# Optimization experiments

Hardware: AMD Instinct MI355X
Metric: run time of the kernel (lower is better)

The kernel has to match this reference:

```python
import jax, jax.numpy as jnp
import numpy as np

JITTER_NOISE = 0.01  # matches init_kwargs jitter_noise


def setup_inputs() -> dict:
    key = jax.random.key(0)
    k1, k2, k3 = jax.random.split(key, 3)
    G, T, D, E = 8, 4096, 2048, 64
    token_inputs = jax.random.normal(k1, (G, T, D), dtype=jnp.float32)
    noise = jax.random.uniform(k2, (G, T, D), dtype=jnp.float32)  # U[0,1), rescaled in reference
    weight = jax.random.normal(k3, (E, D), dtype=jnp.float32) * 0.02  # nn.init.normal_(std=0.02)
    bias = jnp.zeros((E,), dtype=jnp.float32)
    return {"token_inputs": token_inputs, "noise": noise, "weight": weight,
            "bias": bias, "expert_capacity": 128}


def reference(token_inputs, noise, weight, bias, expert_capacity):
    # Jitter: torch uniform_(1 - j, 1 + j) applied multiplicatively
    x = token_inputs * (1.0 - JITTER_NOISE + 2.0 * JITTER_NOISE * noise)
    # Router logits: Linear(dim -> num_experts)
    logits = jnp.einsum('gtd,ed->gte', x, weight) + bias  # [G, T, E]
    probs = jax.nn.softmax(logits, axis=-1)
    # ignore_padding_tokens: zero logits of all-zero tokens
    padding_mask = (jnp.sum(jnp.abs(x), axis=-1) > 0)[..., None]  # [G, T, 1]
    masked_logits = logits * padding_mask
    # Router z-loss on (masked) logits
    log_z = jax.nn.logsumexp(masked_logits, axis=-1)  # [G, T]
    G, T, _ = masked_logits.shape
    z_loss = jnp.sum(log_z ** 2) / (G * T)
    return probs, masked_logits, z_loss
```

## Files before the change

### kernel.cpp

```cpp
#include <hip/hip_runtime.h>
#include <math.h>

#define G_   8
#define T_   4096
#define D_   2048
#define E_   64
#define ROWS (G_*T_)
#define BM   64
#define BK   32
#define NIT  (D_/BK)

__global__ __launch_bounds__(256) void router_kernel(
    const float* __restrict__ tok,
    const float* __restrict__ noi,
    const float* __restrict__ wgt,
    const float* __restrict__ bias,
    float* __restrict__ probs,
    float* __restrict__ masked,
    float* __restrict__ zloss)
{
    __shared__ float xs[BK][BM];
    __shared__ float ws[BK][E_];
    __shared__ float abs_row[BM];
    __shared__ float zred[4];

    const int tid  = threadIdx.x;
    const int lrow = tid >> 2;
    const int lc   = tid & 3;
    const int ty   = tid >> 4;
    const int tx   = tid & 15;
    const size_t row0 = (size_t)blockIdx.x * BM;

    const float* tbase = tok + (row0 + (size_t)lrow) * D_ + lc * 4;
    const float* nbase = noi + (row0 + (size_t)lrow) * D_ + lc * 4;
    const float* wbase = wgt + (size_t)lrow * D_ + lc * 4;

    float acc[4][4];
#pragma unroll
    for (int i = 0; i < 4; ++i)
#pragma unroll
        for (int j = 0; j < 4; ++j) acc[i][j] = 0.f;
    float absacc = 0.f;

    float4 a0 = *(const float4*)(tbase +  0);
    float4 a1 = *(const float4*)(tbase + 16);
    float4 n0 = *(const float4*)(nbase +  0);
    float4 n1 = *(const float4*)(nbase + 16);
    float4 w0 = *(const float4*)(wbase +  0);
    float4 w1 = *(const float4*)(wbase + 16);

    for (int it = 0; it < NIT; ++it) {
        float4 x0, x1;
        x0.x = a0.x * (0.99f + 0.02f * n0.x);
        x0.y = a0.y * (0.99f + 0.02f * n0.y);
        x0.z = a0.z * (0.99f + 0.02f * n0.z);
        x0.w = a0.w * (0.99f + 0.02f * n0.w);
        x1.x = a1.x * (0.99f + 0.02f * n1.x);
        x1.y = a1.y * (0.99f + 0.02f * n1.y);
        x1.z = a1.z * (0.99f + 0.02f * n1.z);
        x1.w = a1.w * (0.99f + 0.02f * n1.w);
        absacc += fabsf(x0.x) + fabsf(x0.y) + fabsf(x0.z) + fabsf(x0.w)
                + fabsf(x1.x) + fabsf(x1.y) + fabsf(x1.z) + fabsf(x1.w);

        xs[lc*4+0 ][lrow] = x0.x;  xs[lc*4+1 ][lrow] = x0.y;
        xs[lc*4+2 ][lrow] = x0.z;  xs[lc*4+3 ][lrow] = x0.w;
        xs[lc*4+16][lrow] = x1.x;  xs[lc*4+17][lrow] = x1.y;
        xs[lc*4+18][lrow] = x1.z;  xs[lc*4+19][lrow] = x1.w;
        ws[lc*4+0 ][lrow] = w0.x;  ws[lc*4+1 ][lrow] = w0.y;
        ws[lc*4+2 ][lrow] = w0.z;  ws[lc*4+3 ][lrow] = w0.w;
        ws[lc*4+16][lrow] = w1.x;  ws[lc*4+17][lrow] = w1.y;
        ws[lc*4+18][lrow] = w1.z;  ws[lc*4+19][lrow] = w1.w;
        __syncthreads();

        {
            int knext = (it + 1 < NIT) ? (it + 1) * BK : it * BK;
            a0 = *(const float4*)(tbase + knext);
            a1 = *(const float4*)(tbase + knext + 16);
            n0 = *(const float4*)(nbase + knext);
            n1 = *(const float4*)(nbase + knext + 16);
            w0 = *(const float4*)(wbase + knext);
            w1 = *(const float4*)(wbase + knext + 16);
        }

#pragma unroll 8
        for (int k = 0; k < BK; ++k) {
            float4 av = *(const float4*)&xs[k][ty*4];
            float4 bv = *(const float4*)&ws[k][tx*4];
            float aa[4] = {av.x, av.y, av.z, av.w};
            float bb[4] = {bv.x, bv.y, bv.z, bv.w};
#pragma unroll
            for (int i = 0; i < 4; ++i)
#pragma unroll
                for (int j = 0; j < 4; ++j)
                    acc[i][j] = fmaf(aa[i], bb[j], acc[i][j]);
        }
        __syncthreads();
    }

    absacc += __shfl_xor(absacc, 1);
    absacc += __shfl_xor(absacc, 2);
    if (lc == 0) abs_row[lrow] = absacc;
    __syncthreads();

    float bj[4];
#pragma unroll
    for (int j = 0; j < 4; ++j) bj[j] = bias[tx*4 + j];

    float zpart = 0.f;
#pragma unroll
    for (int i = 0; i < 4; ++i) {
        const size_t gr = row0 + (size_t)(ty*4 + i);
        float l[4];
#pragma unroll
        for (int j = 0; j < 4; ++j) l[j] = acc[i][j] + bj[j];

        float m = fmaxf(fmaxf(l[0], l[1]), fmaxf(l[2], l[3]));
        m = fmaxf(m, __shfl_xor(m, 1));
        m = fmaxf(m, __shfl_xor(m, 2));
        m = fmaxf(m, __shfl_xor(m, 4));
        m = fmaxf(m, __shfl_xor(m, 8));

        float e[4]; float s = 0.f;
#pragma unroll
        for (int j = 0; j < 4; ++j) { e[j] = expf(l[j] - m); s += e[j]; }
        s += __shfl_xor(s, 1);
        s += __shfl_xor(s, 2);
        s += __shfl_xor(s, 4);
        s += __shfl_xor(s, 8);
        const float rs = 1.f / s;

        float4 pv = { e[0]*rs, e[1]*rs, e[2]*rs, e[3]*rs };
        *(float4*)(probs + gr * E_ + tx*4) = pv;

        const float msk = (abs_row[ty*4 + i] > 0.f) ? 1.f : 0.f;
        float ml[4];
#pragma unroll
        for (int j = 0; j < 4; ++j) ml[j] = l[j] * msk;
        float4 mv = { ml[0], ml[1], ml[2], ml[3] };
        *(float4*)(masked + gr * E_ + tx*4) = mv;

        float mm = fmaxf(fmaxf(ml[0], ml[1]), fmaxf(ml[2], ml[3]));
        mm = fmaxf(mm, __shfl_xor(mm, 1));
        mm = fmaxf(mm, __shfl_xor(mm, 2));
        mm = fmaxf(mm, __shfl_xor(mm, 4));
        mm = fmaxf(mm, __shfl_xor(mm, 8));
        float ss = 0.f;
#pragma unroll
        for (int j = 0; j < 4; ++j) ss += expf(ml[j] - mm);
        ss += __shfl_xor(ss, 1);
        ss += __shfl_xor(ss, 2);
        ss += __shfl_xor(ss, 4);
        ss += __shfl_xor(ss, 8);
        if (tx == 0) {
            const float lse = mm + logf(ss);
            zpart += lse * lse;
        }
    }

    zpart += __shfl_xor(zpart, 32);
    zpart += __shfl_xor(zpart, 16);
    zpart += __shfl_xor(zpart, 8);
    zpart += __shfl_xor(zpart, 4);
    zpart += __shfl_xor(zpart, 2);
    zpart += __shfl_xor(zpart, 1);
    if ((tid & 63) == 0) zred[tid >> 6] = zpart;
    __syncthreads();
    if (tid == 0) {
        const float z = (zred[0] + zred[1]) + (zred[2] + zred[3]);
        atomicAdd(zloss, z * (1.0f / (float)ROWS));
    }
}

extern "C" void kernel_launch(void* const* d_in, const int* in_sizes, int n_in,
                              void* d_out, int out_size, void* d_ws, size_t ws_size,
                              hipStream_t stream) {
    (void)in_sizes; (void)n_in; (void)ws_size; (void)out_size; (void)d_ws;
    const float* tok  = (const float*)d_in[0];
    const float* noi  = (const float*)d_in[1];
    const float* wgt  = (const float*)d_in[2];
    const float* bias = (const float*)d_in[3];

    float* probs  = (float*)d_out;
    float* masked = probs + (size_t)ROWS * E_;
    float* zloss  = probs + 2 * (size_t)ROWS * E_;

    hipMemsetAsync(zloss, 0, sizeof(float), stream);

    dim3 grid(ROWS / BM);
    dim3 block(256);
    router_kernel<<<grid, block, 0, stream>>>(tok, noi, wgt, bias, probs, masked, zloss);
}
```

Before: 565.0 us.

## Split-K router GEMM with larger 256-row tiles and separate softmax epilogue

Splits the reduction dimension into four slices, each handled by a block computing a 256x64 tile with an 8x8 per-thread register tile. Partial logits and per-row abs sums are accumulated with atomics into the output buffer and a workspace. A second kernel then applies bias, softmax, masking and the z-loss. This raises arithmetic intensity and per-thread ILP, at the cost of float atomics, extra memsets and a second pass over the logits.

```diff
diff --git a/kernel.cpp b/kernel.cpp
--- a/kernel.cpp
+++ b/kernel.cpp
@@ -1,192 +1,221 @@
 #include <hip/hip_runtime.h>
 #include <math.h>
 
-#define G_   8
-#define T_   4096
-#define D_   2048
-#define E_   64
-#define ROWS (G_*T_)
-#define BM   64
-#define BK   32
-#define NIT  (D_/BK)
-
-__global__ __launch_bounds__(256) void router_kernel(
+#define D_    2048
+#define E_    64
+#define ROWS  32768
+#define BM    256
+#define BK    32
+#define KSL   4
+#define KD    (D_/KSL)
+#define NIT   (KD/BK)
+#define XS    260
+#define WSTR  68
+
+__global__ __launch_bounds__(256, 2) void router_gemm(
     const float* __restrict__ tok,
     const float* __restrict__ noi,
     const float* __restrict__ wgt,
+    float* __restrict__ lacc,
+    float* __restrict__ absrow)
+{
+    __shared__ float xs[BK][XS];
+    __shared__ float wsh[BK][WSTR];
+
+    const int tid  = threadIdx.x;
+    const int lane = tid & 63;
+    const int wv   = tid >> 6;
+    const int rowblk = (int)blockIdx.x >> 2;
+    const int ks     = (int)blockIdx.x & 3;
+    const size_t row0 = (size_t)rowblk * BM;
+    const int k0 = ks * KD;
+
+    const int lr  = wv*8 + (lane>>3);
+    const int lko = (lane&7)*4;
+    const float* tptr = tok + (row0 + (size_t)lr)*D_ + (k0 + lko);
+    const float* nptr = noi + (row0 + (size_t)lr)*D_ + (k0 + lko);
+
+    const int we  = tid >> 2;
+    const int wko = (tid & 3) * 8;
+    const float* wptr = wgt + (size_t)we*D_ + (k0 + wko);
+
+    const int ty = tid >> 3;
+    const int tx = tid & 7;
+
+    float acc[8][8];
+#pragma unroll
+    for (int i = 0; i < 8; ++i)
+#pragma unroll
+        for (int j = 0; j < 8; ++j) acc[i][j] = 0.f;
+    float absp[8];
+#pragma unroll
+    for (int p = 0; p < 8; ++p) absp[p] = 0.f;
+
+    float4 ta[8], na[8], wa, wb;
+#pragma unroll
+    for (int p = 0; p < 8; ++p) {
+        ta[p] = *(const float4*)(tptr + (size_t)p*32*D_);
+        na[p] = *(const float4*)(nptr + (size_t)p*32*D_);
+    }
+    wa = *(const float4*)(wptr);
+    wb = *(const float4*)(wptr + 4);
+
+    for (int it = 0; it < NIT; ++it) {
+        __syncthreads();
+
+#pragma unroll
+        for (int p = 0; p < 8; ++p) {
+            const int row = p*32 + lr;
+            const float x0 = ta[p].x * (0.99f + 0.02f * na[p].x);
+            const float x1 = ta[p].y * (0.99f + 0.02f * na[p].y);
+            const float x2 = ta[p].z * (0.99f + 0.02f * na[p].z);
+            const float x3 = ta[p].w * (0.99f + 0.02f * na[p].w);
+            xs[lko+0][row] = x0;
+            xs[lko+1][row] = x1;
+            xs[lko+2][row] = x2;
+            xs[lko+3][row] = x3;
+            absp[p] += fabsf(x0) + fabsf(x1) + fabsf(x2) + fabsf(x3);
+        }
+        {
+            const float* w0 = &wa.x;
+            const float* w1 = &wb.x;
+#pragma unroll
+            for (int j = 0; j < 4; ++j) wsh[wko+j][we]   = w0[j];
+#pragma unroll
+            for (int j = 0; j < 4; ++j) wsh[wko+4+j][we] = w1[j];
+        }
+        __syncthreads();
+
+        {
+            const int itn = (it + 1 < NIT) ? it + 1 : it;
+            const float* tp = tptr + itn*BK;
+            const float* np = nptr + itn*BK;
+            const float* wp = wptr + itn*BK;
+#pragma unroll
+            for (int p = 0; p < 8; ++p) {
+                ta[p] = *(const float4*)(tp + (size_t)p*32*D_);
+                na[p] = *(const float4*)(np + (size_t)p*32*D_);
+            }
+            wa = *(const float4*)(wp);
+            wb = *(const float4*)(wp + 4);
+        }
+
+#pragma unroll 8
+        for (int k = 0; k < BK; ++k) {
+            float4 a0 = *(const float4*)&xs[k][ty*8];
+            float4 a1 = *(const float4*)&xs[k][ty*8+4];
+            float4 b0 = *(const float4*)&wsh[k][tx*8];
+            float4 b1 = *(const float4*)&wsh[k][tx*8+4];
+            float av[8] = {a0.x,a0.y,a0.z,a0.w,a1.x,a1.y,a1.z,a1.w};
+            float bv[8] = {b0.x,b0.y,b0.z,b0.w,b1.x,b1.y,b1.z,b1.w};
+#pragma unroll
+            for (int i = 0; i < 8; ++i)
+#pragma unroll
+                for (int j = 0; j < 8; ++j)
+                    acc[i][j] = fmaf(av[i], bv[j], acc[i][j]);
+        }
+    }
+
+#pragma unroll
+    for (int i = 0; i < 8; ++i) {
+        float* base = lacc + (row0 + (size_t)(ty*8 + i))*E_ + tx*8;
+#pragma unroll
+        for (int j = 0; j < 8; ++j) atomicAdd(base + j, acc[i][j]);
+    }
+
+#pragma unroll
+    for (int p = 0; p < 8; ++p) {
+        float v = absp[p];
+        v += __shfl_xor(v, 1);
+        v += __shfl_xor(v, 2);
+        v += __shfl_xor(v, 4);
+        if ((lane & 7) == 0) atomicAdd(&absrow[row0 + (size_t)(p*32 + lr)], v);
+    }
+}
+
+__global__ __launch_bounds__(256) void router_epi(
     const float* __restrict__ bias,
     float* __restrict__ probs,
-    float* __restrict__ masked,
+    float* __restrict__ lacc,
+    const float* __restrict__ absrow,
     float* __restrict__ zloss)
 {
-    __shared__ float xs[BK][BM];
-    __shared__ float ws[BK][E_];
-    __shared__ float abs_row[BM];
     __shared__ float zred[4];
-
-    const int tid  = threadIdx.x;
-    const int lrow = tid >> 2;
-    const int lc   = tid & 3;
-    const int ty   = tid >> 4;
-    const int tx   = tid & 15;
-    const size_t row0 = (size_t)blockIdx.x * BM;
-
-    const float* tbase = tok + (row0 + (size_t)lrow) * D_ + lc * 4;
-    const float* nbase = noi + (row0 + (size_t)lrow) * D_ + lc * 4;
-    const float* wbase = wgt + (size_t)lrow * D_ + lc * 4;
-
-    float acc[4][4];
-#pragma unroll
-    for (int i = 0; i < 4; ++i)
-#pragma unroll
-        for (int j = 0; j < 4; ++j) acc[i][j] = 0.f;
-    float absacc = 0.f;
-
-    float4 a0 = *(const float4*)(tbase +  0);
-    float4 a1 = *(const float4*)(tbase + 16);
-    float4 n0 = *(const float4*)(nbase +  0);
-    float4 n1 = *(const float4*)(nbase + 16);
-    float4 w0 = *(const float4*)(wbase +  0);
-    float4 w1 = *(const float4*)(wbase + 16);
-
-    for (int it = 0; it < NIT; ++it) {
-        float4 x0, x1;
-        x0.x = a0.x * (0.99f + 0.02f * n0.x);
-        x0.y = a0.y * (0.99f + 0.02f * n0.y);
-        x0.z = a0.z * (0.99f + 0.02f * n0.z);
-        x0.w = a0.w * (0.99f + 0.02f * n0.w);
-        x1.x = a1.x * (0.99f + 0.02f * n1.x);
-        x1.y = a1.y * (0.99f + 0.02f * n1.y);
-        x1.z = a1.z * (0.99f + 0.02f * n1.z);
-        x1.w = a1.w * (0.99f + 0.02f * n1.w);
-        absacc += fabsf(x0.x) + fabsf(x0.y) + fabsf(x0.z) + fabsf(x0.w)
-                + fabsf(x1.x) + fabsf(x1.y) + fabsf(x1.z) + fabsf(x1.w);
-
-        xs[lc*4+0 ][lrow] = x0.x;  xs[lc*4+1 ][lrow] = x0.y;
-        xs[lc*4+2 ][lrow] = x0.z;  xs[lc*4+3 ][lrow] = x0.w;
-        xs[lc*4+16][lrow] = x1.x;  xs[lc*4+17][lrow] = x1.y;
-        xs[lc*4+18][lrow] = x1.z;  xs[lc*4+19][lrow] = x1.w;
-        ws[lc*4+0 ][lrow] = w0.x;  ws[lc*4+1 ][lrow] = w0.y;
-        ws[lc*4+2 ][lrow] = w0.z;  ws[lc*4+3 ][lrow] = w0.w;
-        ws[lc*4+16][lrow] = w1.x;  ws[lc*4+17][lrow] = w1.y;
-        ws[lc*4+18][lrow] = w1.z;  ws[lc*4+19][lrow] = w1.w;
-        __syncthreads();
-
-        {
-            int knext = (it + 1 < NIT) ? (it + 1) * BK : it * BK;
-            a0 = *(const float4*)(tbase + knext);
-            a1 = *(const float4*)(tbase + knext + 16);
-            n0 = *(const float4*)(nbase + knext);
-            n1 = *(const float4*)(nbase + knext + 16);
-            w0 = *(const float4*)(wbase + knext);
-            w1 = *(const float4*)(wbase + knext + 16);
-        }
-
-#pragma unroll 8
-        for (int k = 0; k < BK; ++k) {
-            float4 av = *(const float4*)&xs[k][ty*4];
-            float4 bv = *(const float4*)&ws[k][tx*4];
-            float aa[4] = {av.x, av.y, av.z, av.w};
-            float bb[4] = {bv.x, bv.y, bv.z, bv.w};
-#pragma unroll
-            for (int i = 0; i < 4; ++i)
-#pragma unroll
-                for (int j = 0; j < 4; ++j)
-                    acc[i][j] = fmaf(aa[i], bb[j], acc[i][j]);
-        }
-        __syncthreads();
-    }
-
-    absacc += __shfl_xor(absacc, 1);
-    absacc += __shfl_xor(absacc, 2);
-    if (lc == 0) abs_row[lrow] = absacc;
+    const int tid = threadIdx.x;
+    const int lane = tid & 63;
+    const int wv = tid >> 6;
+    const int r  = tid >> 4;
+    const int tx = tid & 15;
+    const size_t row = (size_t)blockIdx.x*16 + r;
+
+    float4 l4 = *(const float4*)&lacc[row*E_ + tx*4];
+    float l[4] = { l4.x + bias[tx*4+0], l4.y + bias[tx*4+1],
+                   l4.z + bias[tx*4+2], l4.w + bias[tx*4+3] };
+
+    float m = fmaxf(fmaxf(l[0], l[1]), fmaxf(l[2], l[3]));
+    m = fmaxf(m, __shfl_xor(m, 1));
+    m = fmaxf(m, __shfl_xor(m, 2));
+    m = fmaxf(m, __shfl_xor(m, 4));
+    m = fmaxf(m, __shfl_xor(m, 8));
+    float e[4]; float s = 0.f;
+#pragma unroll
+    for (int j = 0; j < 4; ++j) { e[j] = expf(l[j] - m); s += e[j]; }
+    s += __shfl_xor(s, 1);
+    s += __shfl_xor(s, 2);
+    s += __shfl_xor(s, 4);
+    s += __shfl_xor(s, 8);
+    const float rs = 1.f / s;
+    float4 pv = { e[0]*rs, e[1]*rs, e[2]*rs, e[3]*rs };
+    *(float4*)(probs + row*E_ + tx*4) = pv;
+
+    const float msk = (absrow[row] > 0.f) ? 1.f : 0.f;
+    float ml[4] = { l[0]*msk, l[1]*msk, l[2]*msk, l[3]*msk };
+    float4 mv = { ml[0], ml[1], ml[2], ml[3] };
+    *(float4*)(lacc + row*E_ + tx*4) = mv;
+
+    float mm = fmaxf(fmaxf(ml[0], ml[1]), fmaxf(ml[2], ml[3]));
+    mm = fmaxf(mm, __shfl_xor(mm, 1));
+    mm = fmaxf(mm, __shfl_xor(mm, 2));
+    mm = fmaxf(mm, __shfl_xor(mm, 4));
+    mm = fmaxf(mm, __shfl_xor(mm, 8));
+    float ss = 0.f;
+#pragma unroll
+    for (int j = 0; j < 4; ++j) ss += expf(ml[j] - mm);
+    ss += __shfl_xor(ss, 1);
+    ss += __shfl_xor(ss, 2);
+    ss += __shfl_xor(ss, 4);
+    ss += __shfl_xor(ss, 8);
+
+    float zp = 0.f;
+    if (tx == 0) {
+        const float lse = mm + logf(ss);
+        zp = lse * lse;
+    }
+    zp += __shfl_xor(zp, 16);
+    zp += __shfl_xor(zp, 32);
+    if (lane == 0) zred[wv] = zp;
     __syncthreads();
-
-    float bj[4];
-#pragma unroll
-    for (int j = 0; j < 4; ++j) bj[j] = bias[tx*4 + j];
-
-    float zpart = 0.f;
-#pragma unroll
-    for (int i = 0; i < 4; ++i) {
-        const size_t gr = row0 + (size_t)(ty*4 + i);
-        float l[4];
-#pragma unroll
-        for (int j = 0; j < 4; ++j) l[j] = acc[i][j] + bj[j];
-
-        float m = fmaxf(fmaxf(l[0], l[1]), fmaxf(l[2], l[3]));
-        m = fmaxf(m, __shfl_xor(m, 1));
-        m = fmaxf(m, __shfl_xor(m, 2));
-        m = fmaxf(m, __shfl_xor(m, 4));
-        m = fmaxf(m, __shfl_xor(m, 8));
-
-        float e[4]; float s = 0.f;
-#pragma unroll
-        for (int j = 0; j < 4; ++j) { e[j] = expf(l[j] - m); s += e[j]; }
-        s += __shfl_xor(s, 1);
-        s += __shfl_xor(s, 2);
-        s += __shfl_xor(s, 4);
-        s += __shfl_xor(s, 8);
-        const float rs = 1.f / s;
-
-        float4 pv = { e[0]*rs, e[1]*rs, e[2]*rs, e[3]*rs };
-        *(float4*)(probs + gr * E_ + tx*4) = pv;
-
-        const float msk = (abs_row[ty*4 + i] > 0.f) ? 1.f : 0.f;
-        float ml[4];
-#pragma unroll
-        for (int j = 0; j < 4; ++j) ml[j] = l[j] * msk;
-        float4 mv = { ml[0], ml[1], ml[2], ml[3] };
-        *(float4*)(masked + gr * E_ + tx*4) = mv;
-
-        float mm = fmaxf(fmaxf(ml[0], ml[1]), fmaxf(ml[2], ml[3]));
-        mm = fmaxf(mm, __shfl_xor(mm, 1));
-        mm = fmaxf(mm, __shfl_xor(mm, 2));
-        mm = fmaxf(mm, __shfl_xor(mm, 4));
-        mm = fmaxf(mm, __shfl_xor(mm, 8));
-        float ss = 0.f;
-#pragma unroll
-        for (int j = 0; j < 4; ++j) ss += expf(ml[j] - mm);
-        ss += __shfl_xor(ss, 1);
-        ss += __shfl_xor(ss, 2);
-        ss += __shfl_xor(ss, 4);
-        ss += __shfl_xor(ss, 8);
-        if (tx == 0) {
-            const float lse = mm + logf(ss);
-            zpart += lse * lse;
-        }
-    }
-
-    zpart += __shfl_xor(zpart, 32);
-    zpart += __shfl_xor(zpart, 16);
-    zpart += __shfl_xor(zpart, 8);
-    zpart += __shfl_xor(zpart, 4);
-    zpart += __shfl_xor(zpart, 2);
-    zpart += __shfl_xor(zpart, 1);
-    if ((tid & 63) == 0) zred[tid >> 6] = zpart;
-    __syncthreads();
-    if (tid == 0) {
-        const float z = (zred[0] + zred[1]) + (zred[2] + zred[3]);
-        atomicAdd(zloss, z * (1.0f / (float)ROWS));
-    }
+    if (tid == 0)
+        atomicAdd(zloss, (zred[0]+zred[1]+zred[2]+zred[3]) * (1.0f/(float)ROWS));
 }
 
 extern "C" void kernel_launch(void* const* d_in, const int* in_sizes, int n_in,
                               void* d_out, int out_size, void* d_ws, size_t ws_size,
                               hipStream_t stream) {
-    (void)in_sizes; (void)n_in; (void)ws_size; (void)out_size; (void)d_ws;
+    (void)in_sizes; (void)n_in; (void)ws_size; (void)out_size;
     const float* tok  = (const float*)d_in[0];
     const float* noi  = (const float*)d_in[1];
     const float* wgt  = (const float*)d_in[2];
     const float* bias = (const float*)d_in[3];
 
     float* probs  = (float*)d_out;
-    float* masked = probs + (size_t)ROWS * E_;
+    float* lacc   = probs + (size_t)ROWS * E_;
     float* zloss  = probs + 2 * (size_t)ROWS * E_;
-
-    hipMemsetAsync(zloss, 0, sizeof(float), stream);
-
-    dim3 grid(ROWS / BM);
-    dim3 block(256);
-    router_kernel<<<grid, block, 0, stream>>>(tok, noi, wgt, bias, probs, masked, zloss);
+    float* absrow = (float*)d_ws;
+
+    hipMemsetAsync(lacc, 0, ((size_t)ROWS * E_ + 1) * sizeof(float), stream);
+    hipMemsetAsync(absrow, 0, (size_t)ROWS * sizeof(float), stream);
+
+    router_gemm<<<dim3((ROWS/BM)*KSL), dim3(256), 0, stream>>>(tok, noi, wgt, lacc, absrow);
+    router_epi <<<dim3(ROWS/16),       dim3(256), 0, stream>>>(bias, probs, lacc, absrow, zloss);
 }
```

Result: slower. 766.0 us (+35.6%).
